# Kernel tuning notes

Hardware: AMD Instinct MI355X
Metric: run time of the kernel (lower is better)

## Reference

```python
import jax, jax.numpy as jnp
import numpy as np

B, T, D, H = 4, 2048, 1024, 16
DH = D // H

def setup_inputs() -> dict:
    key = jax.random.key(0)
    ks = jax.random.split(key, 8)
    scale = 1.0 / np.sqrt(D)
    return {
        "q": jax.random.normal(ks[0], (B, T, D), dtype=jnp.float32),
        "k": jax.random.normal(ks[1], (B, T, D), dtype=jnp.float32),
        "v": jax.random.normal(ks[2], (B, T, D), dtype=jnp.float32),
        "wq": jax.random.normal(ks[3], (D, D), dtype=jnp.float32) * scale,
        "wk": jax.random.normal(ks[4], (D, D), dtype=jnp.float32) * scale,
        "wv": jax.random.normal(ks[5], (D, D), dtype=jnp.float32) * scale,
        "wo": jax.random.normal(ks[6], (D, D), dtype=jnp.float32) * scale,
        "mask": jnp.tril(jnp.ones((T, T), dtype=bool)),  # causal [Tq,Tk]
    }

def reference(q, k, v, wq, wk, wv, wo, mask):
    Bq, Tq, C = q.shape
    Tk = k.shape[1]
    # nn.Linear(bias=False): y = x @ W.T, W is [out,in]
    qh = (q @ wq.T).reshape(Bq, Tq, H, DH).transpose(0, 2, 1, 3)  # [B,H,Tq,DH]
    kh = (k @ wk.T).reshape(Bq, Tk, H, DH).transpose(0, 2, 1, 3)
    vh = (v @ wv.T).reshape(Bq, Tk, H, DH).transpose(0, 2, 1, 3)
    att = jnp.einsum("bhqd,bhkd->bhqk", qh, kh) / np.sqrt(DH)
    att = jnp.where(mask[None, None, :, :], att, -jnp.inf)
    att = jax.nn.softmax(att, axis=-1)
    out = jnp.einsum("bhqk,bhkd->bhqd", att, vh)
    out = out.transpose(0, 2, 1, 3).reshape(Bq, Tq, C)
    return out @ wo.T
```

## Files before the change

kernel.cpp:

```cpp
#include <hip/hip_runtime.h>
#include <hip/hip_bf16.h>

typedef short bf16x8 __attribute__((ext_vector_type(8)));
typedef float f32x4 __attribute__((ext_vector_type(4)));
typedef float f32x16 __attribute__((ext_vector_type(16)));

#define N_B 4
#define N_T 2048
#define N_D 1024
#define N_H 16
#define N_DH 64

#define Q_SCALE 0.18033688011112042f

__device__ __forceinline__ unsigned short f2bf(float f) {
  union { float f; unsigned int u; } c; c.f = f;
  unsigned int u = c.u;
  return (unsigned short)((u + 0x7FFFu + ((u >> 16) & 1u)) >> 16);
}

__device__ __forceinline__ unsigned cvtpk_bf16(float lo, float hi) {
  unsigned r;
  asm("v_cvt_pk_bf16_f32 %0, %1, %2" : "=v"(r) : "v"(lo), "v"(hi));
  return r;
}

__device__ __forceinline__ void gll16(const unsigned short* g, unsigned short* l) {
  __builtin_amdgcn_global_load_lds(
      (const __attribute__((address_space(1))) unsigned int*)(const void*)g,
      (__attribute__((address_space(3))) unsigned int*)(void*)l, 16, 0, 0);
}

__global__ void cast_all(const float* __restrict__ wq, const float* __restrict__ wk,
                         const float* __restrict__ wv, const float* __restrict__ wo,
                         const float* __restrict__ q, const float* __restrict__ k,
                         const float* __restrict__ v,
                         unsigned short* __restrict__ ws) {
  const int z = blockIdx.z;
  const float* srcs[7] = {wq, wk, wv, wo, q, k, v};
  const int size = (z < 4) ? (N_D * N_D) : (N_B * N_T * N_D);
  const size_t off = (z < 4) ? (size_t)z * (N_D * N_D)
                             : (size_t)4 * (N_D * N_D) + (size_t)(z - 4) * (N_B * N_T * N_D);
  const int i = (blockIdx.x * 256 + threadIdx.x) * 8;
  if (i >= size) return;
  const float* src = srcs[z];
  float4 a = *(const float4*)(src + i);
  float4 b = *(const float4*)(src + i + 4);
  bf16x8 p;
  p[0] = (short)f2bf(a.x); p[1] = (short)f2bf(a.y);
  p[2] = (short)f2bf(a.z); p[3] = (short)f2bf(a.w);
  p[4] = (short)f2bf(b.x); p[5] = (short)f2bf(b.y);
  p[6] = (short)f2bf(b.z); p[7] = (short)f2bf(b.w);
  *(bf16x8*)(ws + off + i) = p;
}

__launch_bounds__(256, 2)
__global__ void proj_qkv(const unsigned short* __restrict__ qb,
                         const unsigned short* __restrict__ kb,
                         const unsigned short* __restrict__ vb,
                         const unsigned short* __restrict__ wq,
                         const unsigned short* __restrict__ wk,
                         const unsigned short* __restrict__ wv,
                         unsigned short* __restrict__ qh,
                         unsigned short* __restrict__ kh,
                         unsigned short* __restrict__ vt) {
  const int z = blockIdx.z;
  const unsigned short* X = (z == 0) ? qb : (z == 1) ? kb : vb;
  const unsigned short* W = (z == 0) ? wq : (z == 1) ? wk : wv;
  unsigned short* O = (z == 0) ? qh : (z == 1) ? kh : vt;

  __shared__ unsigned short lds_a[128 * 64];
  __shared__ unsigned short lds_b[128 * 64];

  const int tid = threadIdx.x;
  const int wave = tid >> 6, lane = tid & 63;
  const int wm = wave >> 1, wn = wave & 1;
  const int lr = lane & 15, lg = lane >> 4;
  const int orig = blockIdx.y * 8 + blockIdx.x;
  const int swz = (orig & 7) * 64 + (orig >> 3);
  const int m0 = (swz >> 3) * 128, n0 = (swz & 7) * 128;
  const int sw = (lr & 7) << 4;

  f32x4 acc[4][4] = {};

  for (int k0 = 0; k0 < N_D; k0 += 64) {
    __syncthreads();
#pragma unroll
    for (int it = 0; it < 4; ++it) {
      int c = it * 256 + tid;
      int row = c >> 3;
      int sb = ((c & 7) * 16) ^ ((row & 7) << 4);
      gll16(&X[(size_t)(m0 + row) * N_D + k0 + (sb >> 1)], &lds_a[c * 8]);
      gll16(&W[(size_t)(n0 + row) * N_D + k0 + (sb >> 1)], &lds_b[c * 8]);
    }
    __syncthreads();

#pragma unroll
    for (int kk = 0; kk < 2; ++kk) {
      bf16x8 af[4], bfr[4];
      const int cb = (lg * 16 + kk * 64);
#pragma unroll
      for (int m = 0; m < 4; ++m)
        af[m] = *(bf16x8*)&lds_a[(wm * 64 + m * 16 + lr) * 64 + ((cb ^ sw) >> 1)];
#pragma unroll
      for (int n = 0; n < 4; ++n)
        bfr[n] = *(bf16x8*)&lds_b[(wn * 64 + n * 16 + lr) * 64 + ((cb ^ sw) >> 1)];
#pragma unroll
      for (int m = 0; m < 4; ++m)
#pragma unroll
        for (int n = 0; n < 4; ++n)
          acc[m][n] = __builtin_amdgcn_mfma_f32_16x16x32_bf16(af[m], bfr[n], acc[m][n], 0, 0, 0);
    }
  }

  const float osc = (z == 0) ? Q_SCALE : 1.0f;
#pragma unroll
  for (int m = 0; m < 4; ++m)
#pragma unroll
    for (int n = 0; n < 4; ++n)
#pragma unroll
      for (int r = 0; r < 4; ++r) {
        int row = m0 + wm * 64 + m * 16 + lg * 4 + r;
        int col = n0 + wn * 64 + n * 16 + lr;
        int b = row >> 11, t = row & (N_T - 1);
        int hh = col >> 6, dh = col & 63;
        unsigned short val = f2bf(acc[m][n][r] * osc);
        if (z < 2)
          O[(((size_t)(b * N_H + hh)) * N_T + t) * N_DH + dh] = val;
        else
          O[(((size_t)(b * N_H + hh)) * N_DH + dh) * N_T + t] = val;
      }
}

__launch_bounds__(256, 2)
__global__ void proj_out(const unsigned short* __restrict__ A,
                         const unsigned short* __restrict__ W,
                         float* __restrict__ out) {
  __shared__ unsigned short lds_a[128 * 64];
  __shared__ unsigned short lds_b[128 * 64];

  const int tid = threadIdx.x;
  const int wave = tid >> 6, lane = tid & 63;
  const int wm = wave >> 1, wn = wave & 1;
  const int lr = lane & 15, lg = lane >> 4;
  const int orig = blockIdx.y * 8 + blockIdx.x;
  const int swz = (orig & 7) * 64 + (orig >> 3);
  const int m0 = (swz >> 3) * 128, n0 = (swz & 7) * 128;
  const int sw = (lr & 7) << 4;

  f32x4 acc[4][4] = {};

  for (int k0 = 0; k0 < N_D; k0 += 64) {
    __syncthreads();
#pragma unroll
    for (int it = 0; it < 4; ++it) {
      int c = it * 256 + tid;
      int row = c >> 3;
      int sb = ((c & 7) * 16) ^ ((row & 7) << 4);
      gll16(&A[(size_t)(m0 + row) * N_D + k0 + (sb >> 1)], &lds_a[c * 8]);
      gll16(&W[(size_t)(n0 + row) * N_D + k0 + (sb >> 1)], &lds_b[c * 8]);
    }
    __syncthreads();

#pragma unroll
    for (int kk = 0; kk < 2; ++kk) {
      bf16x8 af[4], bfr[4];
      const int cb = (lg * 16 + kk * 64);
#pragma unroll
      for (int m = 0; m < 4; ++m)
        af[m] = *(bf16x8*)&lds_a[(wm * 64 + m * 16 + lr) * 64 + ((cb ^ sw) >> 1)];
#pragma unroll
      for (int n = 0; n < 4; ++n)
        bfr[n] = *(bf16x8*)&lds_b[(wn * 64 + n * 16 + lr) * 64 + ((cb ^ sw) >> 1)];
#pragma unroll
      for (int m = 0; m < 4; ++m)
#pragma unroll
        for (int n = 0; n < 4; ++n)
          acc[m][n] = __builtin_amdgcn_mfma_f32_16x16x32_bf16(af[m], bfr[n], acc[m][n], 0, 0, 0);
    }
  }

#pragma unroll
  for (int m = 0; m < 4; ++m)
#pragma unroll
    for (int n = 0; n < 4; ++n)
#pragma unroll
      for (int r = 0; r < 4; ++r) {
        int row = m0 + wm * 64 + m * 16 + lg * 4 + r;
        int col = n0 + wn * 64 + n * 16 + lr;
        out[(size_t)row * N_D + col] = acc[m][n][r];
      }
}

__launch_bounds__(256, 2)
__global__ void attn(const unsigned short* __restrict__ qh,
                     const unsigned short* __restrict__ kh,
                     const unsigned short* __restrict__ vt,
                     unsigned short* __restrict__ att) {
  __shared__ unsigned short k_lds[2][64 * 64];
  __shared__ unsigned short v_lds[2][64 * 64];

  const int tid = threadIdx.x;
  const int wave = tid >> 6, lane = tid & 63;
  const int l31 = lane & 31, hi = lane >> 5;
  const int L = (int)blockIdx.x + (int)blockIdx.y * 8;
  const int bh = (L & 7) | ((L >> 6) << 3);
  const int px = (L >> 3) & 7;
  const size_t base = (size_t)bh * N_T * N_DH;
  const unsigned short* Q = qh + base;
  const unsigned short* K = kh + base;
  const unsigned short* V = vt + base;
  const int b = bh >> 4, h = bh & 15;
  const int swr = (l31 & 7) << 4;

  bf16x8 ones;
#pragma unroll
  for (int j = 0; j < 8; ++j) ones[j] = (short)0x3F80;

  auto stage = [&](int buf, int kb2) {
    const int kk0 = kb2 * 64;
#pragma unroll
    for (int it = 0; it < 2; ++it) {
      int c = it * 256 + tid;
      int row = c >> 3;
      int sb = ((c & 7) * 16) ^ ((row & 7) << 4);
      gll16(&K[(size_t)(kk0 + row) * N_DH + (sb >> 1)], &k_lds[buf][c * 8]);
      gll16(&V[(size_t)row * N_T + kk0 + (sb >> 1)], &v_lds[buf][c * 8]);
    }
  };

  for (int half = 0; half < 2; ++half) {
    const int qt = half ? (15 - px) : px;
    const int q0 = qt * 128;
    const int q0w = q0 + wave * 32;

    bf16x8 qf[4];
#pragma unroll
    for (int i = 0; i < 4; ++i)
      qf[i] = *(const bf16x8*)&Q[(size_t)(q0w + l31) * N_DH + i * 16 + hi * 8];

    float m_r = -INFINITY;
    f32x16 l_acc = {};
    f32x16 o0 = {}, o1 = {};

    const int nkb = 2 * qt + 2;

    __syncthreads();
    stage(0, 0);

    for (int kb = 0; kb < nkb; ++kb) {
      const int cur = kb & 1;
      __syncthreads();
      if (kb + 1 < nkb) stage(cur ^ 1, kb + 1);

      const unsigned short* kt_ = k_lds[cur];
      const unsigned short* vt_ = v_lds[cur];

      const int kgb0 = kb * 64;
      const int kgb1 = kb * 64 + 32;
      if (kgb0 > q0w + 31) continue;
      const bool a1 = (kgb1 <= q0w + 31);

      f32x16 s0 = {}, s1 = {};
      __builtin_amdgcn_s_setprio(1);
#pragma unroll
      for (int i = 0; i < 4; ++i) {
        bf16x8 kf = *(const bf16x8*)&kt_[l31 * 64 + (((i * 32 + hi * 16) ^ swr) >> 1)];
        s0 = __builtin_amdgcn_mfma_f32_32x32x16_bf16(kf, qf[i], s0, 0, 0, 0);
      }
      if (a1) {
#pragma unroll
        for (int i = 0; i < 4; ++i) {
          bf16x8 kf = *(const bf16x8*)&kt_[(32 + l31) * 64 + (((i * 32 + hi * 16) ^ swr) >> 1)];
          s1 = __builtin_amdgcn_mfma_f32_32x32x16_bf16(kf, qf[i], s1, 0, 0, 0);
        }
      }
      __builtin_amdgcn_s_setprio(0);

      if (kgb0 == q0w) {
#pragma unroll
        for (int j = 0; j < 16; ++j)
          if ((j & 3) + 8 * (j >> 2) + 4 * hi > l31) s0[j] = -1e30f;
      }
      if (a1 && kgb1 == q0w) {
#pragma unroll
        for (int j = 0; j < 16; ++j)
          if ((j & 3) + 8 * (j >> 2) + 4 * hi > l31) s1[j] = -1e30f;
      }

      float mx = s0[0];
#pragma unroll
      for (int j = 1; j < 16; ++j) mx = fmaxf(mx, s0[j]);
      if (a1) {
#pragma unroll
        for (int j = 0; j < 16; ++j) mx = fmaxf(mx, s1[j]);
      }
      mx = fmaxf(mx, __shfl_xor(mx, 32));
      if (__any(mx > m_r + 8.0f)) {
        float mn = fmaxf(m_r, mx);
        float al = exp2f(m_r - mn);
        m_r = mn;
#pragma unroll
        for (int j = 0; j < 16; ++j) {
          float aj = __shfl(al, (j & 3) + 8 * (j >> 2) + 4 * hi);
          o0[j] *= aj; o1[j] *= aj; l_acc[j] *= aj;
        }
      }

#pragma unroll
      for (int j = 0; j < 16; ++j) s0[j] = exp2f(s0[j] - m_r);
      if (a1) {
#pragma unroll
        for (int j = 0; j < 16; ++j) s1[j] = exp2f(s1[j] - m_r);
      }

      {
        unsigned t01 = cvtpk_bf16(s0[0], s0[1]),   t45 = cvtpk_bf16(s0[4], s0[5]);
        unsigned t23 = cvtpk_bf16(s0[2], s0[3]),   t67 = cvtpk_bf16(s0[6], s0[7]);
        unsigned u01 = cvtpk_bf16(s0[8], s0[9]),   u45 = cvtpk_bf16(s0[12], s0[13]);
        unsigned u23 = cvtpk_bf16(s0[10], s0[11]), u67 = cvtpk_bf16(s0[14], s0[15]);
        unsigned x01 = __shfl_xor(t01, 32), x45 = __shfl_xor(t45, 32);
        unsigned x23 = __shfl_xor(t23, 32), x67 = __shfl_xor(t67, 32);
        unsigned y01 = __shfl_xor(u01, 32), y45 = __shfl_xor(u45, 32);
        unsigned y23 = __shfl_xor(u23, 32), y67 = __shfl_xor(u67, 32);
        union { unsigned u[4]; bf16x8 v; } pa0, pa1;
        pa0.u[0] = hi ? x45 : t01;  pa0.u[1] = hi ? x67 : t23;
        pa0.u[2] = hi ? t45 : x01;  pa0.u[3] = hi ? t67 : x23;
        pa1.u[0] = hi ? y45 : u01;  pa1.u[1] = hi ? y67 : u23;
        pa1.u[2] = hi ? u45 : y01;  pa1.u[3] = hi ? u67 : y23;

        const int c0 = ((hi * 16) ^ swr) >> 1;
        const int c1 = ((32 + hi * 16) ^ swr) >> 1;
        bf16x8 v00 = *(const bf16x8*)&vt_[l31 * 64 + c0];
        bf16x8 v01 = *(const bf16x8*)&vt_[(32 + l31) * 64 + c0];
        bf16x8 v10 = *(const bf16x8*)&vt_[l31 * 64 + c1];
        bf16x8 v11 = *(const bf16x8*)&vt_[(32 + l31) * 64 + c1];

        __builtin_amdgcn_s_setprio(1);
        o0 = __builtin_amdgcn_mfma_f32_32x32x16_bf16(pa0.v, v00, o0, 0, 0, 0);
        o1 = __builtin_amdgcn_mfma_f32_32x32x16_bf16(pa0.v, v01, o1, 0, 0, 0);
        o0 = __builtin_amdgcn_mfma_f32_32x32x16_bf16(pa1.v, v10, o0, 0, 0, 0);
        o1 = __builtin_amdgcn_mfma_f32_32x32x16_bf16(pa1.v, v11, o1, 0, 0, 0);
        l_acc = __builtin_amdgcn_mfma_f32_32x32x16_bf16(pa0.v, ones, l_acc, 0, 0, 0);
        l_acc = __builtin_amdgcn_mfma_f32_32x32x16_bf16(pa1.v, ones, l_acc, 0, 0, 0);
        __builtin_amdgcn_s_setprio(0);
      }

      if (a1) {
        unsigned t01 = cvtpk_bf16(s1[0], s1[1]),   t45 = cvtpk_bf16(s1[4], s1[5]);
        unsigned t23 = cvtpk_bf16(s1[2], s1[3]),   t67 = cvtpk_bf16(s1[6], s1[7]);
        unsigned u01 = cvtpk_bf16(s1[8], s1[9]),   u45 = cvtpk_bf16(s1[12], s1[13]);
        unsigned u23 = cvtpk_bf16(s1[10], s1[11]), u67 = cvtpk_bf16(s1[14], s1[15]);
        unsigned x01 = __shfl_xor(t01, 32), x45 = __shfl_xor(t45, 32);
        unsigned x23 = __shfl_xor(t23, 32), x67 = __shfl_xor(t67, 32);
        unsigned y01 = __shfl_xor(u01, 32), y45 = __shfl_xor(u45, 32);
        unsigned y23 = __shfl_xor(u23, 32), y67 = __shfl_xor(u67, 32);
        union { unsigned u[4]; bf16x8 v; } pb0, pb1;
        pb0.u[0] = hi ? x45 : t01;  pb0.u[1] = hi ? x67 : t23;
        pb0.u[2] = hi ? t45 : x01;  pb0.u[3] = hi ? t67 : x23;
        pb1.u[0] = hi ? y45 : u01;  pb1.u[1] = hi ? y67 : u23;
        pb1.u[2] = hi ? u45 : y01;  pb1.u[3] = hi ? u67 : y23;

        const int c0 = ((64 + hi * 16) ^ swr) >> 1;
        const int c1 = ((96 + hi * 16) ^ swr) >> 1;
        bf16x8 v00 = *(const bf16x8*)&vt_[l31 * 64 + c0];
        bf16x8 v01 = *(const bf16x8*)&vt_[(32 + l31) * 64 + c0];
        bf16x8 v10 = *(const bf16x8*)&vt_[l31 * 64 + c1];
        bf16x8 v11 = *(const bf16x8*)&vt_[(32 + l31) * 64 + c1];

        __builtin_amdgcn_s_setprio(1);
        o0 = __builtin_amdgcn_mfma_f32_32x32x16_bf16(pb0.v, v00, o0, 0, 0, 0);
        o1 = __builtin_amdgcn_mfma_f32_32x32x16_bf16(pb0.v, v01, o1, 0, 0, 0);
        o0 = __builtin_amdgcn_mfma_f32_32x32x16_bf16(pb1.v, v10, o0, 0, 0, 0);
        o1 = __builtin_amdgcn_mfma_f32_32x32x16_bf16(pb1.v, v11, o1, 0, 0, 0);
        l_acc = __builtin_amdgcn_mfma_f32_32x32x16_bf16(pb0.v, ones, l_acc, 0, 0, 0);
        l_acc = __builtin_amdgcn_mfma_f32_32x32x16_bf16(pb1.v, ones, l_acc, 0, 0, 0);
        __builtin_amdgcn_s_setprio(0);
      }
    }

#pragma unroll
    for (int j = 0; j < 16; ++j) {
      float inv = 1.0f / l_acc[j];
      int t = q0w + (j & 3) + 8 * (j >> 2) + 4 * hi;
      size_t rowb = ((size_t)(b * N_T + t)) * N_D + h * 64 + l31;
      att[rowb]      = f2bf(o0[j] * inv);
      att[rowb + 32] = f2bf(o1[j] * inv);
    }
  }
}

extern "C" void kernel_launch(void* const* d_in, const int* in_sizes, int n_in,
                              void* d_out, int out_size, void* d_ws, size_t ws_size,
                              hipStream_t stream) {
  (void)in_sizes; (void)n_in; (void)out_size; (void)ws_size;
  const float* q  = (const float*)d_in[0];
  const float* k  = (const float*)d_in[1];
  const float* v  = (const float*)d_in[2];
  const float* wq = (const float*)d_in[3];
  const float* wk = (const float*)d_in[4];
  const float* wv = (const float*)d_in[5];
  const float* wo = (const float*)d_in[6];
  float* out = (float*)d_out;

  unsigned short* ws = (unsigned short*)d_ws;
  const size_t W_ELEMS = (size_t)N_D * N_D;
  const size_t T_ELEMS = (size_t)N_B * N_T * N_D;
  unsigned short* wqb = ws;
  unsigned short* wkb = wqb + W_ELEMS;
  unsigned short* wvb = wkb + W_ELEMS;
  unsigned short* wob = wvb + W_ELEMS;
  unsigned short* qb  = wob + W_ELEMS;
  unsigned short* kb  = qb + T_ELEMS;
  unsigned short* vb  = kb + T_ELEMS;
  unsigned short* qhb = vb + T_ELEMS;
  unsigned short* khb = qhb + T_ELEMS;
  unsigned short* vtb = khb + T_ELEMS;
  unsigned short* att = qb;

  cast_all<<<dim3(4096, 1, 7), 256, 0, stream>>>(wq, wk, wv, wo, q, k, v, ws);
  proj_qkv<<<dim3(8, 64, 3), 256, 0, stream>>>(qb, kb, vb, wqb, wkb, wvb, qhb, khb, vtb);
  attn<<<dim3(8, N_B * N_H), 256, 0, stream>>>(qhb, khb, vtb, att);
  proj_out<<<dim3(8, 64), 256, 0, stream>>>(att, wob, out);
}
```

Before: 205.0 us.

## Process both causal query tiles in one pass sharing K/V staging

Instead of looping over two query tiles (px and 15-px) sequentially and restaging K/V for each, the block keeps both tiles' Q fragments and accumulators live and walks the K/V range once. Each staged K/V block feeds both tiles, so global loads and LDS staging for the shorter tile's prefix are no longer repeated. The cost is roughly doubled accumulator and Q register usage, which may lower occupancy or cause spills.

Result: slower. 211.2 us (+3.0%).

```diff
diff --git a/kernel.cpp b/kernel.cpp
--- a/kernel.cpp
+++ b/kernel.cpp
@@ -217,6 +217,22 @@
 #pragma unroll
   for (int j = 0; j < 8; ++j) ones[j] = (short)0x3F80;
 
+  const int qtA = px;
+  const int qtB = 15 - px;
+  const int q0wA = qtA * 128 + wave * 32;
+  const int q0wB = qtB * 128 + wave * 32;
+
+  bf16x8 qfA[4], qfB[4];
+#pragma unroll
+  for (int i = 0; i < 4; ++i) {
+    qfA[i] = *(const bf16x8*)&Q[(size_t)(q0wA + l31) * N_DH + i * 16 + hi * 8];
+    qfB[i] = *(const bf16x8*)&Q[(size_t)(q0wB + l31) * N_DH + i * 16 + hi * 8];
+  }
+
+  float mA = -INFINITY, mB = -INFINITY;
+  f32x16 lA = {}, lB = {};
+  f32x16 oA0 = {}, oA1 = {}, oB0 = {}, oB1 = {};
+
   auto stage = [&](int buf, int kb2) {
     const int kk0 = kb2 * 64;
 #pragma unroll
@@ -229,36 +245,23 @@
     }
   };
 
-  for (int half = 0; half < 2; ++half) {
-    const int qt = half ? (15 - px) : px;
-    const int q0 = qt * 128;
-    const int q0w = q0 + wave * 32;
-
-    bf16x8 qf[4];
-#pragma unroll
-    for (int i = 0; i < 4; ++i)
-      qf[i] = *(const bf16x8*)&Q[(size_t)(q0w + l31) * N_DH + i * 16 + hi * 8];
-
-    float m_r = -INFINITY;
-    f32x16 l_acc = {};
-    f32x16 o0 = {}, o1 = {};
-
-    const int nkb = 2 * qt + 2;
-
+  const int nkb = 2 * qtB + 2;
+
+  stage(0, 0);
+
+  for (int kb = 0; kb < nkb; ++kb) {
+    const int cur = kb & 1;
     __syncthreads();
-    stage(0, 0);
-
-    for (int kb = 0; kb < nkb; ++kb) {
-      const int cur = kb & 1;
-      __syncthreads();
-      if (kb + 1 < nkb) stage(cur ^ 1, kb + 1);
-
-      const unsigned short* kt_ = k_lds[cur];
-      const unsigned short* vt_ = v_lds[cur];
-
+    if (kb + 1 < nkb) stage(cur ^ 1, kb + 1);
+
+    const unsigned short* kt_ = k_lds[cur];
+    const unsigned short* vt_ = v_lds[cur];
+
+    auto tile = [&](int q0w, const bf16x8 (&qf)[4], float& m_r, f32x16& l_acc,
+                    f32x16& o0, f32x16& o1) {
       const int kgb0 = kb * 64;
       const int kgb1 = kb * 64 + 32;
-      if (kgb0 > q0w + 31) continue;
+      if (kgb0 > q0w + 31) return;
       const bool a1 = (kgb1 <= q0w + 31);
 
       f32x16 s0 = {}, s1 = {};
@@ -377,16 +380,23 @@
         l_acc = __builtin_amdgcn_mfma_f32_32x32x16_bf16(pb1.v, ones, l_acc, 0, 0, 0);
         __builtin_amdgcn_s_setprio(0);
       }
-    }
-
-#pragma unroll
-    for (int j = 0; j < 16; ++j) {
-      float inv = 1.0f / l_acc[j];
-      int t = q0w + (j & 3) + 8 * (j >> 2) + 4 * hi;
-      size_t rowb = ((size_t)(b * N_T + t)) * N_D + h * 64 + l31;
-      att[rowb]      = f2bf(o0[j] * inv);
-      att[rowb + 32] = f2bf(o1[j] * inv);
-    }
+    };
+
+    tile(q0wB, qfB, mB, lB, oB0, oB1);
+    tile(q0wA, qfA, mA, lA, oA0, oA1);
+  }
+
+#pragma unroll
+  for (int j = 0; j < 16; ++j) {
+    int ridx = (j & 3) + 8 * (j >> 2) + 4 * hi;
+    float invA = 1.0f / lA[j];
+    float invB = 1.0f / lB[j];
+    size_t rowbA = ((size_t)(b * N_T + q0wA + ridx)) * N_D + h * 64 + l31;
+    size_t rowbB = ((size_t)(b * N_T + q0wB + ridx)) * N_D + h * 64 + l31;
+    att[rowbA]      = f2bf(oA0[j] * invA);
+    att[rowbA + 32] = f2bf(oA1[j] * invA);
+    att[rowbB]      = f2bf(oB0[j] * invB);
+    att[rowbB + 32] = f2bf(oB1[j] * invB);
   }
 }
 
```
